# Kernel optimization log

Hardware: AMD Instinct MI355X
Metric: run time of the kernel (lower is better)

The kernel has to match this reference:

```python
import jax, jax.numpy as jnp
import numpy as np
import math

D = 768
H = 12
HD = D // H  # 64


def setup_inputs() -> dict:
    key = jax.random.key(0)
    ks = jax.random.split(key, 8)
    B, S = 32, 127
    desc = jax.random.normal(ks[0], (B, S, D), dtype=jnp.float32)
    nv = jax.random.normal(ks[1], (B, S + 1, D), dtype=jnp.float32)
    def xavier(k, shape):
        fan_in, fan_out = shape[1], shape[0]
        gain = 1.0 / math.sqrt(2.0)
        limit = gain * math.sqrt(6.0 / (fan_in + fan_out))
        return jax.random.uniform(k, shape, jnp.float32, -limit, limit)
    Wq = xavier(ks[2], (D, D)); bq = jnp.zeros((D,), jnp.float32)
    Wk = xavier(ks[3], (D, D)); bk = jnp.zeros((D,), jnp.float32)
    Wv = xavier(ks[4], (D, D)); bv = jnp.zeros((D,), jnp.float32)
    # attn_proj: Linear(3*head_dim, 1)
    Wa = xavier(ks[5], (1, 3 * HD))[0]  # [3*HD]
    ba = jnp.zeros((), jnp.float32)
    return {
        "desc_embeddings": desc,
        "name_value_embeddings": nv,
        "Wq": Wq, "bq": bq, "Wk": Wk, "bk": bk, "Wv": Wv, "bv": bv,
        "Wa": Wa, "ba": ba,
    }


def _forward(desc_embeddings, name_value_embeddings, Wq, bq, Wk, bk, Wv, bv, Wa, ba):
    B, new_seq, _ = name_value_embeddings.shape
    S = new_seq - 1

    # adjacency: var-var all ones, CLS->Var row = 1, Var->CLS col = 0, CLS->CLS = 0
    adj = jnp.zeros((new_seq, new_seq), jnp.float32)
    adj = adj.at[1:, 1:].set(1.0)
    adj = adj.at[0, 1:].set(1.0)
    adj = jnp.broadcast_to(adj, (B, new_seq, new_seq))

    # q,k,v: [B, H, new_seq, HD]
    def proj(W, b):
        y = name_value_embeddings @ W.T + b
        return y.reshape(B, new_seq, H, HD).transpose(0, 2, 1, 3)
    q = proj(Wq, bq); k = proj(Wk, bk); v = proj(Wv, bv)

    # attn_proj weight split: [q_part | k_part | edge_part], each [HD]
    wq_a, wk_a, we_a = Wa[:HD], Wa[HD:2 * HD], Wa[2 * HD:]

    # q/k scalar contributions per (b,h,i) and (b,h,j)
    lq = jnp.einsum('bhid,d->bhi', q, wq_a)  # [B,H,new_seq]
    lk = jnp.einsum('bhjd,d->bhj', k, wk_a)  # [B,H,new_seq]

    # edge_attr[b,i,j] per head h (head slice of concat[node_i_desc, node_j_desc]):
    # edge vector = concat(desc_i, desc_j)[h*HD:(h+1)*HD] viewed as [H, HD] of 2D dims.
    # concat(desc_i, desc_j) has 2D dims -> reshaped to [H, HD] means head h takes
    # slice [h*HD:(h+1)*HD] of the 2D-dim concat. Heads 0..H/2-1 come from desc_i,
    # heads H/2..H-1 come from desc_j. Compute edge dot with we_a accordingly.
    # desc_full[b,t] : [B,S,D]. Build per-head contributions:
    # for h < H//2: edge slice = desc_i[h*HD:(h+1)*HD]  -> depends only on i
    # for h >= H//2: edge slice = desc_j[(h-H//2)*HD:(h-H//2+1)*HD] -> depends only on j
    desc_heads = desc_embeddings.reshape(B, S, H // 2, 2 * HD)  # wrong split; do directly
    # Direct: per head h, slice indices into the 2D concat vector
    dh = desc_embeddings.reshape(B, S, H, HD)  # desc split into H chunks of HD (covers D = H*HD)
    # concat(desc_i,desc_j) reshaped to [H,HD]: heads 0..H/2-1 use dh_i[:, :, h],
    # heads H/2..H-1 use dh_j[:, :, h - H/2]
    e_dot = jnp.einsum('bshd,d->bsh', dh, jnp.broadcast_to(we_a, (HD,)))  # placeholder, recompute per head below
    # per-head edge scalar contribution for var-var edges:
    ei = jnp.einsum('bshd,d->bhs', dh, we_a)  # contribution if head slice comes from desc at position s
    Hh = H // 2
    # var-var logits edge part: for h<Hh depends on i; for h>=Hh depends on j
    le_i = ei[:, :Hh, :]   # [B,Hh,S] depends on i (row)
    le_j = ei[:, Hh:, :]   # [B,Hh,S] depends on j (col)

    # CLS edges: cls_edge_attr = concat(desc, desc) at position t (the var index)
    # row 0 (CLS->var j): edge = concat(desc_j, desc_j) -> head h slice:
    #   h<Hh: dh_j[h]; h>=Hh: dh_j[h-Hh]  -> scalar ei[b,h,j] with h mapped
    e_cls = jnp.concatenate([ei[:, :Hh, :], ei[:, :Hh, :]], axis=1) * 0  # init
    e_cls = jnp.concatenate([le_i, le_i], axis=1)  # [B,H,S]: head h<Hh uses dh[h], h>=Hh uses dh[h-Hh]
    # note ei[:, :Hh] corresponds to dh chunks 0..Hh-1 ; for h>=Hh slice is dh[h-Hh] -> same le_i

    # Assemble full logits [B,H,new_seq,new_seq]
    logits = lq[:, :, :, None] + lk[:, :, None, :]
    # edge contributions (only where adj==1; edge_attr zeroed elsewhere by mask mult)
    edge = jnp.zeros((B, H, new_seq, new_seq), jnp.float32)
    # var-var block [1:,1:]
    ev = jnp.zeros((B, H, S, S), jnp.float32)
    ev = ev + jnp.pad(le_i, ((0, 0), (0, Hh), (0, 0)))[:, :, :, None] * 0  # keep shapes
    ev_i = jnp.concatenate([le_i, jnp.zeros_like(le_j)], axis=1)  # h<Hh: i-dependent
    ev_j = jnp.concatenate([jnp.zeros_like(le_i), le_j], axis=1)  # h>=Hh: j-dependent
    ev = ev_i[:, :, :, None] + ev_j[:, :, None, :]  # [B,H,S,S]
    edge = edge.at[:, :, 1:, 1:].set(ev)
    # CLS row (0, 1:): cls_edge = concat(desc_j,desc_j); j = column var
    edge = edge.at[:, :, 0, 1:].set(e_cls)
    # CLS col (1:, 0): cls_edge = concat(desc_i,desc_i) BUT adj[:,1:,0]=0 so edge_attr
    # multiplied by adj -> zero; also masked out. edge stays 0, but torch zeroes it too.
    # mask edge by adjacency (edge_attr *= adj)
    edge = edge * adj[:, None, :, :]
    logits = logits + edge + ba

    mask = (adj[:, None, :, :] == 0).astype(jnp.float32) * -1e9
    logits = logits + mask
    attn = jax.nn.softmax(logits, axis=-1)  # [B,H,new_seq,new_seq]
    ctx = jnp.einsum('bhij,bhjd->bhid', attn, v)
    basis_outputs = ctx.transpose(0, 2, 1, 3)  # [B,new_seq,H,HD]
    return basis_outputs, attn


def reference(desc_embeddings, name_value_embeddings, Wq, bq, Wk, bk, Wv, bv, Wa, ba):
    return _forward(desc_embeddings, name_value_embeddings, Wq, bq, Wk, bk, Wv, bv, Wa, ba)
```

## Files before the change

### kernel.cpp

```cpp
#include <hip/hip_runtime.h>

#define NB 32
#define NS 128
#define SD 127
#define ND 768
#define NH 12
#define HD 64

__device__ inline float wredSum(float v){
  #pragma unroll
  for (int off=32; off>0; off>>=1) v += __shfl_xor(v, off);
  return v;
}
__device__ inline float wredMax(float v){
  #pragma unroll
  for (int off=32; off>0; off>>=1) v = fmaxf(v, __shfl_xor(v, off));
  return v;
}

__global__ __launch_bounds__(256)
void fold_k(const float* __restrict__ Wk, const float* __restrict__ bk,
            const float* __restrict__ Wa, float* __restrict__ uk,
            float* __restrict__ bkdot){
  int blk = blockIdx.x;
  int h = blk/12, cb = blk%12;
  int t = threadIdx.x;
  int c0 = t & 63, dg = t >> 6;
  const float* base = Wk + (size_t)(h*HD + dg*16)*ND + cb*64 + c0;
  float acc = 0.f;
  #pragma unroll
  for (int i=0;i<16;++i) acc += base[(size_t)i*ND] * Wa[64 + dg*16 + i];
  __shared__ float red[4][64];
  red[dg][c0] = acc;
  __syncthreads();
  if (dg==0) uk[h*ND + cb*64 + c0] = red[0][c0]+red[1][c0]+red[2][c0]+red[3][c0];
  if (blk==0 && t < NH){
    float a = 0.f;
    for (int d=0; d<64; ++d) a += bk[t*HD+d]*Wa[64+d];
    bkdot[t] = a;
  }
}

__global__ __launch_bounds__(256)
void lk_ei(const float* __restrict__ nv, const float* __restrict__ desc,
           const float* __restrict__ uk, const float* __restrict__ bkdot,
           const float* __restrict__ Wa,
           float* __restrict__ lk, float* __restrict__ ei){
  __shared__ float sh[ND];
  int blk = blockIdx.x;
  int wave = threadIdx.x >> 6, lane = threadIdx.x & 63;
  if (blk < NB*NS){
    int b = blk >> 7, j = blk & 127;
    const float* row = nv + (size_t)blk * ND;
    for (int c = threadIdx.x; c < ND; c += 256) sh[c] = row[c];
    __syncthreads();
    #pragma unroll
    for (int hh=0; hh<3; ++hh){
      int h = wave*3 + hh;
      float acc = 0.f;
      #pragma unroll
      for (int k=0; k<12; ++k) acc += sh[lane+64*k]*uk[h*ND + lane+64*k];
      acc = wredSum(acc);
      if (lane==0) lk[(b*NH + h)*NS + j] = acc + bkdot[h];
    }
  } else {
    int bs = blk - NB*NS;
    int b = bs / SD, s = bs % SD;
    float wea = Wa[128 + lane];
    const float* row = desc + (size_t)bs * ND;
    #pragma unroll
    for (int hh=0; hh<3; ++hh){
      int h = wave + hh*4;
      float v = row[h*HD + lane] * wea;
      v = wredSum(v);
      if (lane==0) ei[(b*NH + h)*NS + s] = v;
    }
  }
}

__global__ __launch_bounds__(128)
void softmax_k(const float* __restrict__ lk, const float* __restrict__ ei,
               float* __restrict__ w, float* __restrict__ wT){
  int bh = blockIdx.x;
  int b = bh / NH, h = bh % NH;
  int t = threadIdx.x, wave = t >> 6, lane = t & 63;
  const float* lkrow = lk + bh*NS;
  const float* eirow = ei + (b*NH + (wave==0 ? (h%6) : h))*NS;
  float g = (wave==0) ? 1.f : (h>=6 ? 1.f : 0.f);
  float x0 = (lane>=1) ? lkrow[lane] + g*eirow[lane-1] : -3.0e38f;
  float x1 = lkrow[lane+64] + g*eirow[lane+63];
  float mm = wredMax(fmaxf(x0,x1));
  float e0 = (lane>=1) ? __expf(x0-mm) : 0.f;
  float e1 = __expf(x1-mm);
  float s  = wredSum(e0+e1);
  float inv = 1.f/s;
  float v0 = e0*inv, v1 = e1*inv;
  w[(bh*2+wave)*NS + lane]      = v0;
  w[(bh*2+wave)*NS + lane+64]   = v1;
  int r = h*2 + wave;
  wT[(b*NS + lane)*24 + r]      = v0;
  wT[(b*NS + lane+64)*24 + r]   = v1;
}

__global__ __launch_bounds__(192)
void m_kernel(const float* __restrict__ nv, const float* __restrict__ wT,
              float* __restrict__ m_part){
  int blk = blockIdx.x;
  int b = blk >> 2, jg = blk & 3;
  int t = threadIdx.x;
  __shared__ float wld[32][24];
  for (int i=t; i<32*24; i+=192) ((float*)wld)[i] = wT[(size_t)(b*NS + jg*32)*24 + i];
  __syncthreads();
  const float4* nvb = (const float4*)(nv + ((size_t)b*NS + jg*32)*ND);
  float4 acc[24];
  #pragma unroll
  for (int r=0; r<24; ++r) acc[r] = make_float4(0.f,0.f,0.f,0.f);
  #pragma unroll 2
  for (int jj=0; jj<32; ++jj){
    float4 x = nvb[jj*192 + t];
    #pragma unroll
    for (int r=0; r<24; ++r){
      float wr = wld[jj][r];
      acc[r].x += wr*x.x; acc[r].y += wr*x.y;
      acc[r].z += wr*x.z; acc[r].w += wr*x.w;
    }
  }
  #pragma unroll
  for (int r=0; r<24; ++r){
    ((float4*)(m_part + ((size_t)(b*24 + r)*4 + jg)*ND))[t] = acc[r];
  }
}

__global__ __launch_bounds__(256)
void proj_write(const float* __restrict__ m_part, const float* __restrict__ Wv,
                const float* __restrict__ bv, const float* __restrict__ w,
                float* __restrict__ out){
  int bh = blockIdx.x;
  int b = bh / NH, h = bh % NH;
  int t = threadIdx.x, wave = t >> 6, lane = t & 63;
  __shared__ float msum[2][ND];
  __shared__ float wrow[2][NS];
  __shared__ float cvec[2][HD];
  wrow[t>>7][t&127] = w[(size_t)bh*2*NS + t];
  for (int i=t; i<2*ND; i+=256){
    int rl = (i >= ND);
    int c  = i - rl*ND;
    const float* mp = m_part + ((size_t)(b*24 + h*2 + rl)*4)*ND + c;
    msum[rl][c] = mp[0] + mp[ND] + mp[2*ND] + mp[3*ND];
  }
  __syncthreads();
  #pragma unroll 4
  for (int dd=0; dd<16; ++dd){
    int d = wave*16 + dd;
    const float* wvr = Wv + (size_t)(h*HD + d)*ND;
    float p0=0.f, p1=0.f;
    #pragma unroll
    for (int k=0; k<12; ++k){
      float wv = wvr[lane + 64*k];
      p0 += wv*msum[0][lane + 64*k];
      p1 += wv*msum[1][lane + 64*k];
    }
    p0 = wredSum(p0); p1 = wredSum(p1);
    if (lane==0){
      float bb = bv[h*HD + d];
      cvec[0][d] = p0 + bb;
      cvec[1][d] = p1 + bb;
    }
  }
  __syncthreads();
  float4* ao = (float4*)(out + (size_t)NB*NS*ND + (size_t)bh*NS*NS);
  for (int idx=t; idx<4096; idx+=256){
    int i = idx>>5, q = idx&31;
    const float* src = (i==0) ? wrow[0] : wrow[1];
    float4 v = { src[q*4], src[q*4+1], src[q*4+2], src[q*4+3] };
    ao[idx] = v;
  }
  float* bo = out + (size_t)b*NS*ND + h*HD;
  for (int idx=t; idx<2048; idx+=256){
    int i = idx>>4, q = idx&15;
    const float* src = (i==0) ? cvec[0] : cvec[1];
    float4 v = { src[q*4], src[q*4+1], src[q*4+2], src[q*4+3] };
    *(float4*)(bo + (size_t)i*ND + q*4) = v;
  }
}

extern "C" void kernel_launch(void* const* d_in, const int* in_sizes, int n_in,
                              void* d_out, int out_size, void* d_ws, size_t ws_size,
                              hipStream_t stream) {
  const float* desc = (const float*)d_in[0];
  const float* nv   = (const float*)d_in[1];
  const float* Wk   = (const float*)d_in[4];
  const float* bk   = (const float*)d_in[5];
  const float* Wv   = (const float*)d_in[6];
  const float* bv   = (const float*)d_in[7];
  const float* Wa   = (const float*)d_in[8];
  float* out = (float*)d_out;
  float* ws  = (float*)d_ws;

  float* uk     = ws;
  float* bkdot  = ws + 9216;
  float* ei     = ws + 9232;
  float* lkbuf  = ws + 58384;
  float* wbuf   = ws + 107536;
  float* wT     = ws + 205840;
  float* m_part = ws + 304144;

  fold_k    <<<144,  256, 0, stream>>>(Wk, bk, Wa, uk, bkdot);
  lk_ei     <<<8160, 256, 0, stream>>>(nv, desc, uk, bkdot, Wa, lkbuf, ei);
  softmax_k <<<384,  128, 0, stream>>>(lkbuf, ei, wbuf, wT);
  m_kernel  <<<128,  192, 0, stream>>>(nv, wT, m_part);
  proj_write<<<384,  256, 0, stream>>>(m_part, Wv, bv, wbuf, out);
}
```

Before: 143.0 us.

## Fuse softmax into weighted-sum kernel and recompute softmax rows in projection

Removes the standalone softmax kernel. Each block of the weighted-sum kernel now recomputes the softmax for its batch in shared memory, and the projection kernel recomputes its two attention rows from lk/ei, so no w/wT buffers pass through global memory. The sequence is split into 8 chunks instead of 4, giving 256 blocks instead of 128, and the projection uses 512 threads. This drops one launch and some global traffic, at the cost of redundant softmax work (8x per batch) and more partial sums to reduce.

New measurement: 139.8 us. -2.2%, faster.

```diff
diff --git a/kernel.cpp b/kernel.cpp
--- a/kernel.cpp
+++ b/kernel.cpp
@@ -78,80 +78,99 @@
   }
 }
 
-__global__ __launch_bounds__(128)
-void softmax_k(const float* __restrict__ lk, const float* __restrict__ ei,
-               float* __restrict__ w, float* __restrict__ wT){
-  int bh = blockIdx.x;
-  int b = bh / NH, h = bh % NH;
+__global__ __launch_bounds__(256)
+void msoft(const float* __restrict__ nv, const float* __restrict__ lk,
+           const float* __restrict__ ei, float* __restrict__ m_part){
+  int blk = blockIdx.x;
+  int b = blk >> 3, jg = blk & 7;
   int t = threadIdx.x, wave = t >> 6, lane = t & 63;
-  const float* lkrow = lk + bh*NS;
-  const float* eirow = ei + (b*NH + (wave==0 ? (h%6) : h))*NS;
-  float g = (wave==0) ? 1.f : (h>=6 ? 1.f : 0.f);
-  float x0 = (lane>=1) ? lkrow[lane] + g*eirow[lane-1] : -3.0e38f;
-  float x1 = lkrow[lane+64] + g*eirow[lane+63];
-  float mm = wredMax(fmaxf(x0,x1));
-  float e0 = (lane>=1) ? __expf(x0-mm) : 0.f;
-  float e1 = __expf(x1-mm);
-  float s  = wredSum(e0+e1);
-  float inv = 1.f/s;
-  float v0 = e0*inv, v1 = e1*inv;
-  w[(bh*2+wave)*NS + lane]      = v0;
-  w[(bh*2+wave)*NS + lane+64]   = v1;
-  int r = h*2 + wave;
-  wT[(b*NS + lane)*24 + r]      = v0;
-  wT[(b*NS + lane+64)*24 + r]   = v1;
-}
-
-__global__ __launch_bounds__(192)
-void m_kernel(const float* __restrict__ nv, const float* __restrict__ wT,
-              float* __restrict__ m_part){
-  int blk = blockIdx.x;
-  int b = blk >> 2, jg = blk & 3;
-  int t = threadIdx.x;
-  __shared__ float wld[32][24];
-  for (int i=t; i<32*24; i+=192) ((float*)wld)[i] = wT[(size_t)(b*NS + jg*32)*24 + i];
-  __syncthreads();
-  const float4* nvb = (const float4*)(nv + ((size_t)b*NS + jg*32)*ND);
-  float4 acc[24];
-  #pragma unroll
-  for (int r=0; r<24; ++r) acc[r] = make_float4(0.f,0.f,0.f,0.f);
-  #pragma unroll 2
-  for (int jj=0; jj<32; ++jj){
-    float4 x = nvb[jj*192 + t];
-    #pragma unroll
-    for (int r=0; r<24; ++r){
-      float wr = wld[jj][r];
-      acc[r].x += wr*x.x; acc[r].y += wr*x.y;
-      acc[r].z += wr*x.z; acc[r].w += wr*x.w;
-    }
-  }
-  #pragma unroll
-  for (int r=0; r<24; ++r){
-    ((float4*)(m_part + ((size_t)(b*24 + r)*4 + jg)*ND))[t] = acc[r];
-  }
-}
-
-__global__ __launch_bounds__(256)
+  __shared__ float slk[NH][NS];
+  __shared__ float sei[NH][NS];
+  __shared__ float wf[24][NS];
+  for (int i=t; i<NH*NS; i+=256) ((float*)slk)[i] = lk[(size_t)b*NH*NS + i];
+  for (int i=t; i<NH*NS; i+=256){
+    int h = i >> 7, s = i & 127;
+    sei[h][s] = (s < SD) ? ei[((size_t)b*NH + h)*NS + s] : 0.f;
+  }
+  __syncthreads();
+  #pragma unroll
+  for (int rr=0; rr<6; ++rr){
+    int r = wave*6 + rr;
+    int h = r >> 1, which = r & 1;
+    const float* eirow = (which==0) ? sei[h%6] : sei[h];
+    float g = (which==0) ? 1.f : (h>=6 ? 1.f : 0.f);
+    float x0 = (lane>=1) ? slk[h][lane] + g*eirow[lane-1] : -3.0e38f;
+    float x1 = slk[h][lane+64] + g*eirow[lane+63];
+    float mm = wredMax(fmaxf(x0,x1));
+    float e0 = (lane>=1) ? __expf(x0-mm) : 0.f;
+    float e1 = __expf(x1-mm);
+    float s  = wredSum(e0+e1);
+    float inv = 1.f/s;
+    wf[r][lane]    = e0*inv;
+    wf[r][lane+64] = e1*inv;
+  }
+  __syncthreads();
+  if (t < 192){
+    const float4* nvb = (const float4*)(nv + ((size_t)b*NS + jg*16)*ND);
+    float4 acc[24];
+    #pragma unroll
+    for (int r=0; r<24; ++r) acc[r] = make_float4(0.f,0.f,0.f,0.f);
+    #pragma unroll 2
+    for (int jj=0; jj<16; ++jj){
+      float4 x = nvb[jj*192 + t];
+      int j = jg*16 + jj;
+      #pragma unroll
+      for (int r=0; r<24; ++r){
+        float wr = wf[r][j];
+        acc[r].x += wr*x.x; acc[r].y += wr*x.y;
+        acc[r].z += wr*x.z; acc[r].w += wr*x.w;
+      }
+    }
+    #pragma unroll
+    for (int r=0; r<24; ++r)
+      ((float4*)(m_part + ((size_t)(b*24 + r)*8 + jg)*ND))[t] = acc[r];
+  }
+}
+
+__global__ __launch_bounds__(512)
 void proj_write(const float* __restrict__ m_part, const float* __restrict__ Wv,
-                const float* __restrict__ bv, const float* __restrict__ w,
-                float* __restrict__ out){
+                const float* __restrict__ bv, const float* __restrict__ lk,
+                const float* __restrict__ ei, float* __restrict__ out){
   int bh = blockIdx.x;
   int b = bh / NH, h = bh % NH;
   int t = threadIdx.x, wave = t >> 6, lane = t & 63;
   __shared__ float msum[2][ND];
-  __shared__ float wrow[2][NS];
+  __shared__ float w0[NS], w1[NS];
   __shared__ float cvec[2][HD];
-  wrow[t>>7][t&127] = w[(size_t)bh*2*NS + t];
-  for (int i=t; i<2*ND; i+=256){
+
+  if (wave < 2){
+    const float* lkrow = lk + (size_t)bh*NS;
+    const float* eirow = ei + ((size_t)b*NH + (wave==0 ? (h%6) : h))*NS;
+    float g = (wave==0) ? 1.f : (h>=6 ? 1.f : 0.f);
+    float x0 = (lane>=1) ? lkrow[lane] + g*eirow[lane-1] : -3.0e38f;
+    float x1 = lkrow[lane+64] + g*eirow[lane+63];
+    float mm = wredMax(fmaxf(x0,x1));
+    float e0 = (lane>=1) ? __expf(x0-mm) : 0.f;
+    float e1 = __expf(x1-mm);
+    float s  = wredSum(e0+e1);
+    float inv = 1.f/s;
+    float* wd = wave ? w1 : w0;
+    wd[lane]    = e0*inv;
+    wd[lane+64] = e1*inv;
+  }
+  for (int i=t; i<2*ND; i+=512){
     int rl = (i >= ND);
     int c  = i - rl*ND;
-    const float* mp = m_part + ((size_t)(b*24 + h*2 + rl)*4)*ND + c;
-    msum[rl][c] = mp[0] + mp[ND] + mp[2*ND] + mp[3*ND];
-  }
-  __syncthreads();
-  #pragma unroll 4
-  for (int dd=0; dd<16; ++dd){
-    int d = wave*16 + dd;
+    const float* mp = m_part + ((size_t)(b*24 + h*2 + rl)*8)*ND + c;
+    float s = 0.f;
+    #pragma unroll
+    for (int g8=0; g8<8; ++g8) s += mp[(size_t)g8*ND];
+    msum[rl][c] = s;
+  }
+  __syncthreads();
+  #pragma unroll
+  for (int dd=0; dd<8; ++dd){
+    int d = wave*8 + dd;
     const float* wvr = Wv + (size_t)(h*HD + d)*ND;
     float p0=0.f, p1=0.f;
     #pragma unroll
@@ -169,14 +188,14 @@
   }
   __syncthreads();
   float4* ao = (float4*)(out + (size_t)NB*NS*ND + (size_t)bh*NS*NS);
-  for (int idx=t; idx<4096; idx+=256){
+  for (int idx=t; idx<4096; idx+=512){
     int i = idx>>5, q = idx&31;
-    const float* src = (i==0) ? wrow[0] : wrow[1];
+    const float* src = (i==0) ? w0 : w1;
     float4 v = { src[q*4], src[q*4+1], src[q*4+2], src[q*4+3] };
     ao[idx] = v;
   }
   float* bo = out + (size_t)b*NS*ND + h*HD;
-  for (int idx=t; idx<2048; idx+=256){
+  for (int idx=t; idx<2048; idx+=512){
     int i = idx>>4, q = idx&15;
     const float* src = (i==0) ? cvec[0] : cvec[1];
     float4 v = { src[q*4], src[q*4+1], src[q*4+2], src[q*4+3] };
@@ -201,13 +220,10 @@
   float* bkdot  = ws + 9216;
   float* ei     = ws + 9232;
   float* lkbuf  = ws + 58384;
-  float* wbuf   = ws + 107536;
-  float* wT     = ws + 205840;
-  float* m_part = ws + 304144;
+  float* m_part = ws + 107536;
 
   fold_k    <<<144,  256, 0, stream>>>(Wk, bk, Wa, uk, bkdot);
   lk_ei     <<<8160, 256, 0, stream>>>(nv, desc, uk, bkdot, Wa, lkbuf, ei);
-  softmax_k <<<384,  128, 0, stream>>>(lkbuf, ei, wbuf, wT);
-  m_kernel  <<<128,  192, 0, stream>>>(nv, wT, m_part);
-  proj_write<<<384,  256, 0, stream>>>(m_part, Wv, bv, wbuf, out);
-}
+  msoft     <<<256,  256, 0, stream>>>(nv, lkbuf, ei, m_part);
+  proj_write<<<384,  512, 0, stream>>>(m_part, Wv, bv, lkbuf, ei, out);
+}
```
